# Optimization experiments

Hardware: AMD Instinct MI355X
Metric: run time of the kernel (lower is better)

Reference implementation:

```python
import jax, jax.numpy as jnp
import numpy as np

N, K, NB, C, L, H = 10000, 32, 64, 128, 3, 64  # atoms, neighbors, basis, channels, num l-orders, MLP hidden
AVG_AGGREGATE_NUM = 10.0
LN_EPS = 1e-5
MAX_ELEM = 300


def setup_inputs() -> dict:
    key = jax.random.key(0)
    ks = jax.random.split(key, 12)
    return {
        'atomic_numbers': jax.random.randint(ks[0], (N,), 0, MAX_ELEM),
        'edge_vec': jax.random.normal(ks[1], (N, K, 3), jnp.float32),
        'f_sparse_idx_node': jax.random.randint(ks[2], (N, K), 0, N),
        'attn_mask': jax.random.randint(ks[3], (N, K, 1), 0, 2) == 1,
        'edge_scalars': jax.random.normal(ks[4], (N, K, NB), jnp.float32),
        'src_emb': jax.random.normal(ks[5], (MAX_ELEM, NB), jnp.float32),
        'tgt_emb': jax.random.normal(ks[6], (MAX_ELEM, NB), jnp.float32),
        'W1': jax.random.normal(ks[7], (L, 3 * NB, H), jnp.float32) / np.sqrt(3 * NB),
        'b1': jnp.zeros((L, H), jnp.float32),
        'g1': jnp.ones((L, H), jnp.float32),
        'be1': jnp.zeros((L, H), jnp.float32),
        'W2': jax.random.normal(ks[8], (L, H, H), jnp.float32) / np.sqrt(H),
        'b2': jnp.zeros((L, H), jnp.float32),
        'g2': jnp.ones((L, H), jnp.float32),
        'be2': jnp.zeros((L, H), jnp.float32),
        'W3': jax.random.normal(ks[9], (L, H, C), jnp.float32) / np.sqrt(H),
        'b3': jnp.zeros((L, C), jnp.float32),
    }


def _layer_norm(x, g, b):
    mu = jnp.mean(x, axis=-1, keepdims=True)
    var = jnp.var(x, axis=-1, keepdims=True)
    return (x - mu) * jax.lax.rsqrt(var + LN_EPS) * g + b


def _sph_harmonics(unit):
    """e3nn real spherical harmonics l=0,1,2, normalization='norm' (unit input vecs)."""
    x, y, z = unit[..., 0], unit[..., 1], unit[..., 2]
    s3 = float(np.sqrt(3.0))
    y0 = jnp.ones_like(x)[..., None]                       # (N,K,1)
    y1 = jnp.stack([y, z, x], axis=-1)                      # (N,K,3)
    y2 = jnp.stack([s3 * x * y,
                    s3 * y * z,
                    0.5 * (3.0 * z * z - 1.0),
                    s3 * x * z,
                    0.5 * s3 * (x * x - y * y)], axis=-1)   # (N,K,5)
    return [y0, y1, y2]


def reference(atomic_numbers, edge_vec, f_sparse_idx_node, attn_mask, edge_scalars,
              src_emb, tgt_emb, W1, b1, g1, be1, W2, b2, g2, be2, W3, b3):
    n, k = edge_scalars.shape[:2]
    # gather atom-type embeddings: target per center atom, source per neighbor
    tgt = jnp.broadcast_to(tgt_emb[atomic_numbers][:, None, :], (n, k, tgt_emb.shape[1]))
    src = src_emb[atomic_numbers][f_sparse_idx_node]            # (N,K,NB)
    edge_dis_embed = jnp.concatenate([edge_scalars, tgt, src], axis=-1)  # (N,K,3*NB)

    unit = edge_vec / jnp.linalg.norm(edge_vec, axis=-1, keepdims=True)
    sh = _sph_harmonics(unit)

    feats = []
    for i in range(W1.shape[0]):  # small fixed loop over l = 0..lmax
        h = jax.nn.silu(_layer_norm(edge_dis_embed @ W1[i] + b1[i], g1[i], be1[i]))
        h = jax.nn.silu(_layer_norm(h @ W2[i] + b2[i], g2[i], be2[i]))
        h = h @ W3[i] + b3[i]                                   # (N,K,C)
        h = jnp.where(attn_mask, 0.0, h)                        # mask padded neighbors
        feats.append(jnp.einsum('mnd,mnh->mdh', sh[i], h))      # (N,2l+1,C)
    return jnp.concatenate(feats, axis=1) / AVG_AGGREGATE_NUM   # (N,9,C)
```

## Files before the change

kernel.cpp:

```cpp
#include <hip/hip_runtime.h>
#include <hip/hip_bf16.h>


typedef __attribute__((ext_vector_type(8))) short bf16x8;
typedef __attribute__((ext_vector_type(4))) short bf16x4;
typedef __attribute__((ext_vector_type(4))) float f32x4;

__device__ __forceinline__ unsigned short f2bf(float f) {
  __hip_bfloat16 h = __float2bfloat16(f);
  return *reinterpret_cast<unsigned short*>(&h);
}

__global__ __launch_bounds__(256) void prep_weights(
    const float* __restrict__ W1, const float* __restrict__ W2,
    const float* __restrict__ W3, unsigned short* __restrict__ wf) {
  int idx = blockIdx.x * 256 + threadIdx.x;
  if (idx >= 73728) return;
  float val;
  if (idx < 36864) {
    int l = idx / 12288, r = idx % 12288;
    int blk = r >> 9, e = r & 511;
    int Nt = blk / 6, Ks = blk % 6;
    int lane = e >> 3, j = e & 7;
    int k = Ks * 32 + (lane >> 4) * 8 + j;
    int nn = Nt * 16 + (lane & 15);
    val = W1[l * 192 * 64 + k * 64 + nn];
  } else if (idx < 49152) {
    int t = idx - 36864;
    int l = t / 4096, r = t % 4096;
    int blk = r >> 9, e = r & 511;
    int Nt = blk >> 1, Ks = blk & 1;
    int lane = e >> 3, j = e & 7;
    int k = Ks * 32 + (lane >> 4) * 8 + j;
    int nn = Nt * 16 + (lane & 15);
    val = W2[l * 64 * 64 + k * 64 + nn];
  } else {
    int t = idx - 49152;
    int l = t / 8192, r = t % 8192;
    int blk = r >> 9, e = r & 511;
    int Nt = blk >> 1, Ks = blk & 1;
    int lane = e >> 3, j = e & 7;
    int k = Ks * 32 + (lane >> 4) * 8 + j;
    int nn = Nt * 16 + (lane & 15);
    val = W3[l * 64 * 128 + k * 128 + nn];
  }
  wf[idx] = f2bf(val);
}

__global__ __launch_bounds__(256) void sniff_mask(const unsigned int* __restrict__ m,
                                                  int* __restrict__ flag) {
  __shared__ int cOther, cFloat;
  if (threadIdx.x == 0) { cOther = 0; cFloat = 0; }
  __syncthreads();
  int other = 0, flt = 0;
#pragma unroll
  for (int i = 0; i < 8; ++i) {
    unsigned int w = m[threadIdx.x * 8 + i];
    if (w == 0x3F800000u) flt++;
    else if (w > 1u) other++;
  }
  if (other) atomicAdd(&cOther, other);
  if (flt)   atomicAdd(&cFloat, flt);
  __syncthreads();
  if (threadIdx.x == 0) {
    int f;
    if (cOther == 0 && cFloat == 0) f = 0;
    else if (cFloat > cOther)       f = 2;
    else                            f = 1;
    *flag = f;
  }
}

__device__ __forceinline__ bf16x8 cvt8(float4 a, float4 b) {
  bf16x8 r;
  r[0] = (short)f2bf(a.x); r[1] = (short)f2bf(a.y);
  r[2] = (short)f2bf(a.z); r[3] = (short)f2bf(a.w);
  r[4] = (short)f2bf(b.x); r[5] = (short)f2bf(b.y);
  r[6] = (short)f2bf(b.z); r[7] = (short)f2bf(b.w);
  return r;
}

__device__ __forceinline__ void ln2(
    const f32x4 (&acc)[4][2], const float* __restrict__ bb,
    const float* __restrict__ gg, const float* __restrict__ be,
    unsigned short* Uw, int e, int g) {
  float v0[16], v1[16];
  float s0 = 0.f, s20 = 0.f, s1 = 0.f, s21 = 0.f;
#pragma unroll
  for (int mt = 0; mt < 4; ++mt) {
    float4 b4 = *reinterpret_cast<const float4*>(bb + mt * 16 + 4 * g);
    const float* b4p = reinterpret_cast<const float*>(&b4);
#pragma unroll
    for (int i = 0; i < 4; ++i) {
      float x0 = acc[mt][0][i] + b4p[i];
      float x1 = acc[mt][1][i] + b4p[i];
      v0[mt * 4 + i] = x0; s0 += x0; s20 += x0 * x0;
      v1[mt * 4 + i] = x1; s1 += x1; s21 += x1 * x1;
    }
  }
  s0 += __shfl_xor(s0, 16); s20 += __shfl_xor(s20, 16);
  s1 += __shfl_xor(s1, 16); s21 += __shfl_xor(s21, 16);
  s0 += __shfl_xor(s0, 32); s20 += __shfl_xor(s20, 32);
  s1 += __shfl_xor(s1, 32); s21 += __shfl_xor(s21, 32);
  float mu0 = s0 * 0.015625f, mu1 = s1 * 0.015625f;
  float r0 = rsqrtf(s20 * 0.015625f - mu0 * mu0 + 1e-5f);
  float r1 = rsqrtf(s21 * 0.015625f - mu1 * mu1 + 1e-5f);
#pragma unroll
  for (int mt = 0; mt < 4; ++mt) {
    float4 g4 = *reinterpret_cast<const float4*>(gg + mt * 16 + 4 * g);
    float4 e4 = *reinterpret_cast<const float4*>(be + mt * 16 + 4 * g);
    const float* g4p = reinterpret_cast<const float*>(&g4);
    const float* e4p = reinterpret_cast<const float*>(&e4);
    bf16x4 pk0, pk1;
#pragma unroll
    for (int i = 0; i < 4; ++i) {
      float y0 = (v0[mt * 4 + i] - mu0) * r0 * g4p[i] + e4p[i];
      float y1 = (v1[mt * 4 + i] - mu1) * r1 * g4p[i] + e4p[i];
      pk0[i] = (short)f2bf(y0 * __builtin_amdgcn_rcpf(1.0f + __expf(-y0)));
      pk1[i] = (short)f2bf(y1 * __builtin_amdgcn_rcpf(1.0f + __expf(-y1)));
    }
    *reinterpret_cast<bf16x4*>(Uw + e * 72 + mt * 16 + 4 * g) = pk0;
    *reinterpret_cast<bf16x4*>(Uw + (16 + e) * 72 + mt * 16 + 4 * g) = pk1;
  }
}

#define MFMA __builtin_amdgcn_mfma_f32_16x16x32_bf16

__global__ __launch_bounds__(256, 3) void edge_net_kernel(
    const int*   __restrict__ an_arr,
    const float* __restrict__ edge_vec,
    const int*   __restrict__ f_idx,
    const void*  __restrict__ attn_mask,
    const float* __restrict__ edge_scalars,
    const float* __restrict__ src_emb,
    const float* __restrict__ tgt_emb,
    const float* __restrict__ b1, const float* __restrict__ g1, const float* __restrict__ be1,
    const float* __restrict__ b2, const float* __restrict__ g2, const float* __restrict__ be2,
    const float* __restrict__ b3,
    const unsigned short* __restrict__ wf,
    const int* __restrict__ mask_flag,
    float* __restrict__ out, int Nat) {

  __shared__ __align__(16) unsigned short U[4][3200];

  const int tid  = threadIdx.x;
  const int wave = tid >> 6, lane = tid & 63;
  const int e = lane & 15, g = lane >> 4;
  int n = blockIdx.x * 4 + wave;
  const bool valid = (n < Nat);
  if (!valid) n = Nat - 1;

  unsigned short* Uw  = &U[wave][0];
  unsigned short* shB = Uw + 2560;

#pragma unroll
  for (int t = 0; t < 10; ++t) shB[t * 64 + lane] = 0;

  const int mflag = *mask_flag;
  if (g < 2) {
    int k = g * 16 + e;
    bool masked;
    if (mflag == 0)      masked = ((const int*)attn_mask)[n * 32 + k] != 0;
    else if (mflag == 1) masked = ((const unsigned char*)attn_mask)[n * 32 + k] != 0;
    else                 masked = ((const float*)attn_mask)[n * 32 + k] != 0.0f;
    const float mf = masked ? 0.0f : 1.0f;
    const float* ev = edge_vec + ((size_t)n * 32 + k) * 3;
    float ex = ev[0], ey = ev[1], ez = ev[2];
    float rn = rsqrtf(ex * ex + ey * ey + ez * ez);
    float x = ex * rn, y = ey * rn, z = ez * rn;
    const float s3 = 1.7320508075688772f;
    float s[9];
    s[0] = 1.f; s[1] = y; s[2] = z; s[3] = x;
    s[4] = s3 * x * y; s[5] = s3 * y * z; s[6] = 1.5f * z * z - 0.5f;
    s[7] = s3 * x * z; s[8] = 0.5f * s3 * (x * x - y * y);
#pragma unroll
    for (int d = 0; d < 9; ++d) shB[d * 40 + k] = f2bf(s[d] * mf);
  }

  const int an = an_arr[n];
  bf16x8 xf[2][6];
  {
    const float4* t0 = reinterpret_cast<const float4*>(tgt_emb + (size_t)an * 64 + g * 8);
    const float4* t1 = reinterpret_cast<const float4*>(tgt_emb + (size_t)an * 64 + 32 + g * 8);
    bf16x8 xt0 = cvt8(t0[0], t0[1]);
    bf16x8 xt1 = cvt8(t1[0], t1[1]);
#pragma unroll
    for (int nt = 0; nt < 2; ++nt) {
      int k = nt * 16 + e;
      const float* es = edge_scalars + ((size_t)n * 32 + k) * 64 + g * 8;
      const float4* p0 = reinterpret_cast<const float4*>(es);
      const float4* p1 = reinterpret_cast<const float4*>(es + 32);
      xf[nt][0] = cvt8(p0[0], p0[1]);
      xf[nt][1] = cvt8(p1[0], p1[1]);
      xf[nt][2] = xt0;
      xf[nt][3] = xt1;
      int srcA = an_arr[f_idx[n * 32 + k]];
      const float4* s0 = reinterpret_cast<const float4*>(src_emb + (size_t)srcA * 64 + g * 8);
      const float4* s1 = reinterpret_cast<const float4*>(src_emb + (size_t)srcA * 64 + 32 + g * 8);
      xf[nt][4] = cvt8(s0[0], s0[1]);
      xf[nt][5] = cvt8(s1[0], s1[1]);
    }
  }

  bf16x8 bfull = *reinterpret_cast<const bf16x8*>(shB + e * 40 + g * 8);

  for (int l = 0; l < 3; ++l) {
    const unsigned short* w1a = wf + l * 12288;
    const unsigned short* w2a = wf + 36864 + l * 4096;
    const unsigned short* w3a = wf + 49152 + l * 8192;

    f32x4 acc1[4][2];
#pragma unroll
    for (int mt = 0; mt < 4; ++mt)
#pragma unroll
      for (int nt = 0; nt < 2; ++nt) acc1[mt][nt] = (f32x4){0.f, 0.f, 0.f, 0.f};
#pragma unroll
    for (int mt = 0; mt < 4; ++mt)
#pragma unroll
      for (int ks = 0; ks < 6; ++ks) {
        bf16x8 wfr = *reinterpret_cast<const bf16x8*>(w1a + ((mt * 6 + ks) << 9) + lane * 8);
        acc1[mt][0] = MFMA(wfr, xf[0][ks], acc1[mt][0], 0, 0, 0);
        acc1[mt][1] = MFMA(wfr, xf[1][ks], acc1[mt][1], 0, 0, 0);
      }
    ln2(acc1, b1 + l * 64, g1 + l * 64, be1 + l * 64, Uw, e, g);

    bf16x8 hf[2][2];
#pragma unroll
    for (int nt = 0; nt < 2; ++nt)
#pragma unroll
      for (int ks = 0; ks < 2; ++ks)
        hf[nt][ks] = *reinterpret_cast<const bf16x8*>(Uw + (nt * 16 + e) * 72 + ks * 32 + g * 8);
    f32x4 acc2[4][2];
#pragma unroll
    for (int mt = 0; mt < 4; ++mt)
#pragma unroll
      for (int nt = 0; nt < 2; ++nt) acc2[mt][nt] = (f32x4){0.f, 0.f, 0.f, 0.f};
#pragma unroll
    for (int mt = 0; mt < 4; ++mt)
#pragma unroll
      for (int ks = 0; ks < 2; ++ks) {
        bf16x8 wfr = *reinterpret_cast<const bf16x8*>(w2a + ((mt * 2 + ks) << 9) + lane * 8);
        acc2[mt][0] = MFMA(wfr, hf[0][ks], acc2[mt][0], 0, 0, 0);
        acc2[mt][1] = MFMA(wfr, hf[1][ks], acc2[mt][1], 0, 0, 0);
      }
    ln2(acc2, b2 + l * 64, g2 + l * 64, be2 + l * 64, Uw, e, g);

#pragma unroll
    for (int nt = 0; nt < 2; ++nt)
#pragma unroll
      for (int ks = 0; ks < 2; ++ks)
        hf[nt][ks] = *reinterpret_cast<const bf16x8*>(Uw + (nt * 16 + e) * 72 + ks * 32 + g * 8);
    const float* b3l = b3 + l * 128;
    const int lo = l * l, hi = l * l + 2 * l;
    const bool dstore = valid && e >= lo && e <= hi;
    float* op = out + ((size_t)n * 9 + e) * 128 + 4 * g;
    bf16x8 bfr = (e >= lo && e <= hi) ? bfull : (bf16x8)(short)0;
#pragma unroll
    for (int half = 0; half < 2; ++half) {
#pragma unroll
      for (int mt = 0; mt < 4; ++mt) {
        const int mtg = half * 4 + mt;
        f32x4 a30 = (f32x4){0.f, 0.f, 0.f, 0.f};
        f32x4 a31 = (f32x4){0.f, 0.f, 0.f, 0.f};
#pragma unroll
        for (int ks = 0; ks < 2; ++ks) {
          bf16x8 wfr = *reinterpret_cast<const bf16x8*>(w3a + ((mtg * 2 + ks) << 9) + lane * 8);
          a30 = MFMA(wfr, hf[0][ks], a30, 0, 0, 0);
          a31 = MFMA(wfr, hf[1][ks], a31, 0, 0, 0);
        }
        float4 bb = *reinterpret_cast<const float4*>(b3l + mtg * 16 + 4 * g);
        const float* bbp = reinterpret_cast<const float*>(&bb);
#pragma unroll
        for (int i = 0; i < 4; ++i) {
          int row = (mt * 16 + 4 * g + i) * 40;
          Uw[row + e]      = f2bf(a30[i] + bbp[i]);
          Uw[row + 16 + e] = f2bf(a31[i] + bbp[i]);
        }
      }
      asm volatile("s_waitcnt lgkmcnt(0)" ::: "memory");
      __builtin_amdgcn_sched_barrier(0);
#pragma unroll
      for (int mt = 0; mt < 4; ++mt) {
        bf16x8 afr = *reinterpret_cast<const bf16x8*>(Uw + (mt * 16 + e) * 40 + g * 8);
        f32x4 ez = (f32x4){0.f, 0.f, 0.f, 0.f};
        ez = MFMA(afr, bfr, ez, 0, 0, 0);
        if (dstore) {
          float4 v;
          v.x = 0.1f * ez[0]; v.y = 0.1f * ez[1];
          v.z = 0.1f * ez[2]; v.w = 0.1f * ez[3];
          *reinterpret_cast<float4*>(op + (half * 4 + mt) * 16) = v;
        }
      }
      asm volatile("s_waitcnt lgkmcnt(0)" ::: "memory");
      __builtin_amdgcn_sched_barrier(0);
    }
  }
}

extern "C" void kernel_launch(void* const* d_in, const int* in_sizes, int n_in,
                              void* d_out, int out_size, void* d_ws, size_t ws_size,
                              hipStream_t stream) {
  const int*   atomic_numbers = (const int*)  d_in[0];
  const float* edge_vec       = (const float*)d_in[1];
  const int*   f_idx          = (const int*)  d_in[2];
  const void*  attn_mask      = d_in[3];
  const float* edge_scalars   = (const float*)d_in[4];
  const float* src_emb        = (const float*)d_in[5];
  const float* tgt_emb        = (const float*)d_in[6];
  const float* W1  = (const float*)d_in[7];
  const float* b1  = (const float*)d_in[8];
  const float* g1  = (const float*)d_in[9];
  const float* be1 = (const float*)d_in[10];
  const float* W2  = (const float*)d_in[11];
  const float* b2  = (const float*)d_in[12];
  const float* g2  = (const float*)d_in[13];
  const float* be2 = (const float*)d_in[14];
  const float* W3  = (const float*)d_in[15];
  const float* b3  = (const float*)d_in[16];

  unsigned short* wf = (unsigned short*)d_ws;
  int* mask_flag = ((int*)d_ws) + 36864;
  float* out = (float*)d_out;
  const int N = in_sizes[0];

  prep_weights<<<288, 256, 0, stream>>>(W1, W2, W3, wf);
  sniff_mask<<<1, 256, 0, stream>>>((const unsigned int*)attn_mask, mask_flag);
  edge_net_kernel<<<(N + 3) / 4, 256, 0, stream>>>(
      atomic_numbers, edge_vec, f_idx, attn_mask, edge_scalars,
      src_emb, tgt_emb, b1, g1, be1, b2, g2, be2, b3, wf, mask_flag, out, N);
}
```

Before: 150.6 us.

## Keep MLP hidden activations in registers via permuted weight K-layout

```diff
diff --git a/kernel.cpp b/kernel.cpp
--- a/kernel.cpp
+++ b/kernel.cpp
@@ -3,7 +3,6 @@
 
 
 typedef __attribute__((ext_vector_type(8))) short bf16x8;
-typedef __attribute__((ext_vector_type(4))) short bf16x4;
 typedef __attribute__((ext_vector_type(4))) float f32x4;
 
 __device__ __forceinline__ unsigned short f2bf(float f) {
@@ -26,23 +25,27 @@
     int nn = Nt * 16 + (lane & 15);
     val = W1[l * 192 * 64 + k * 64 + nn];
   } else if (idx < 49152) {
-    int t = idx - 36864;
-    int l = t / 4096, r = t % 4096;
+    int t2 = idx - 36864;
+    int l = t2 / 4096, r = t2 % 4096;
     int blk = r >> 9, e = r & 511;
     int Nt = blk >> 1, Ks = blk & 1;
     int lane = e >> 3, j = e & 7;
-    int k = Ks * 32 + (lane >> 4) * 8 + j;
+    int gg = lane >> 4;
+    int t = Ks * 8 + j;
+    int kk = 16 * (t >> 2) + 4 * gg + (t & 3);
     int nn = Nt * 16 + (lane & 15);
-    val = W2[l * 64 * 64 + k * 64 + nn];
+    val = W2[l * 64 * 64 + kk * 64 + nn];
   } else {
-    int t = idx - 49152;
-    int l = t / 8192, r = t % 8192;
+    int t2 = idx - 49152;
+    int l = t2 / 8192, r = t2 % 8192;
     int blk = r >> 9, e = r & 511;
     int Nt = blk >> 1, Ks = blk & 1;
     int lane = e >> 3, j = e & 7;
-    int k = Ks * 32 + (lane >> 4) * 8 + j;
+    int gg = lane >> 4;
+    int t = Ks * 8 + j;
+    int kk = 16 * (t >> 2) + 4 * gg + (t & 3);
     int nn = Nt * 16 + (lane & 15);
-    val = W3[l * 64 * 128 + k * 128 + nn];
+    val = W3[l * 64 * 128 + kk * 128 + nn];
   }
   wf[idx] = f2bf(val);
 }
@@ -83,7 +86,7 @@
 __device__ __forceinline__ void ln2(
     const f32x4 (&acc)[4][2], const float* __restrict__ bb,
     const float* __restrict__ gg, const float* __restrict__ be,
-    unsigned short* Uw, int e, int g) {
+    bf16x8 (&hfo)[2][2], int g) {
   float v0[16], v1[16];
   float s0 = 0.f, s20 = 0.f, s1 = 0.f, s21 = 0.f;
 #pragma unroll
@@ -111,16 +114,16 @@
     float4 e4 = *reinterpret_cast<const float4*>(be + mt * 16 + 4 * g);
     const float* g4p = reinterpret_cast<const float*>(&g4);
     const float* e4p = reinterpret_cast<const float*>(&e4);
-    bf16x4 pk0, pk1;
 #pragma unroll
     for (int i = 0; i < 4; ++i) {
       float y0 = (v0[mt * 4 + i] - mu0) * r0 * g4p[i] + e4p[i];
       float y1 = (v1[mt * 4 + i] - mu1) * r1 * g4p[i] + e4p[i];
-      pk0[i] = (short)f2bf(y0 * __builtin_amdgcn_rcpf(1.0f + __expf(-y0)));
-      pk1[i] = (short)f2bf(y1 * __builtin_amdgcn_rcpf(1.0f + __expf(-y1)));
+      float sl0 = y0 * __builtin_amdgcn_rcpf(1.0f + __expf(-y0));
+      float sl1 = y1 * __builtin_amdgcn_rcpf(1.0f + __expf(-y1));
+      const int t = mt * 4 + i;
+      hfo[0][t >> 3][t & 7] = (short)f2bf(sl0);
+      hfo[1][t >> 3][t & 7] = (short)f2bf(sl1);
     }
-    *reinterpret_cast<bf16x4*>(Uw + e * 72 + mt * 16 + 4 * g) = pk0;
-    *reinterpret_cast<bf16x4*>(Uw + (16 + e) * 72 + mt * 16 + 4 * g) = pk1;
   }
 }
 
@@ -152,6 +155,7 @@
 
   unsigned short* Uw  = &U[wave][0];
   unsigned short* shB = Uw + 2560;
+  unsigned int*   U32 = reinterpret_cast<unsigned int*>(Uw);
 
 #pragma unroll
   for (int t = 0; t < 10; ++t) shB[t * 64 + lane] = 0;
@@ -174,7 +178,7 @@
     s[4] = s3 * x * y; s[5] = s3 * y * z; s[6] = 1.5f * z * z - 0.5f;
     s[7] = s3 * x * z; s[8] = 0.5f * s3 * (x * x - y * y);
 #pragma unroll
-    for (int d = 0; d < 9; ++d) shB[d * 40 + k] = f2bf(s[d] * mf);
+    for (int d = 0; d < 9; ++d) shB[d * 40 + 2 * e + g] = f2bf(s[d] * mf);
   }
 
   const int an = an_arr[n];
@@ -222,14 +226,9 @@
         acc1[mt][0] = MFMA(wfr, xf[0][ks], acc1[mt][0], 0, 0, 0);
         acc1[mt][1] = MFMA(wfr, xf[1][ks], acc1[mt][1], 0, 0, 0);
       }
-    ln2(acc1, b1 + l * 64, g1 + l * 64, be1 + l * 64, Uw, e, g);
-
-    bf16x8 hf[2][2];
-#pragma unroll
-    for (int nt = 0; nt < 2; ++nt)
-#pragma unroll
-      for (int ks = 0; ks < 2; ++ks)
-        hf[nt][ks] = *reinterpret_cast<const bf16x8*>(Uw + (nt * 16 + e) * 72 + ks * 32 + g * 8);
+    bf16x8 hf1[2][2];
+    ln2(acc1, b1 + l * 64, g1 + l * 64, be1 + l * 64, hf1, g);
+
     f32x4 acc2[4][2];
 #pragma unroll
     for (int mt = 0; mt < 4; ++mt)
@@ -240,16 +239,12 @@
 #pragma unroll
       for (int ks = 0; ks < 2; ++ks) {
         bf16x8 wfr = *reinterpret_cast<const bf16x8*>(w2a + ((mt * 2 + ks) << 9) + lane * 8);
-        acc2[mt][0] = MFMA(wfr, hf[0][ks], acc2[mt][0], 0, 0, 0);
-        acc2[mt][1] = MFMA(wfr, hf[1][ks], acc2[mt][1], 0, 0, 0);
+        acc2[mt][0] = MFMA(wfr, hf1[0][ks], acc2[mt][0], 0, 0, 0);
+        acc2[mt][1] = MFMA(wfr, hf1[1][ks], acc2[mt][1], 0, 0, 0);
       }
-    ln2(acc2, b2 + l * 64, g2 + l * 64, be2 + l * 64, Uw, e, g);
-
-#pragma unroll
-    for (int nt = 0; nt < 2; ++nt)
-#pragma unroll
-      for (int ks = 0; ks < 2; ++ks)
-        hf[nt][ks] = *reinterpret_cast<const bf16x8*>(Uw + (nt * 16 + e) * 72 + ks * 32 + g * 8);
+    bf16x8 hf2[2][2];
+    ln2(acc2, b2 + l * 64, g2 + l * 64, be2 + l * 64, hf2, g);
+
     const float* b3l = b3 + l * 128;
     const int lo = l * l, hi = l * l + 2 * l;
     const bool dstore = valid && e >= lo && e <= hi;
@@ -265,16 +260,16 @@
 #pragma unroll
         for (int ks = 0; ks < 2; ++ks) {
           bf16x8 wfr = *reinterpret_cast<const bf16x8*>(w3a + ((mtg * 2 + ks) << 9) + lane * 8);
-          a30 = MFMA(wfr, hf[0][ks], a30, 0, 0, 0);
-          a31 = MFMA(wfr, hf[1][ks], a31, 0, 0, 0);
+          a30 = MFMA(wfr, hf2[0][ks], a30, 0, 0, 0);
+          a31 = MFMA(wfr, hf2[1][ks], a31, 0, 0, 0);
         }
         float4 bb = *reinterpret_cast<const float4*>(b3l + mtg * 16 + 4 * g);
         const float* bbp = reinterpret_cast<const float*>(&bb);
 #pragma unroll
         for (int i = 0; i < 4; ++i) {
-          int row = (mt * 16 + 4 * g + i) * 40;
-          Uw[row + e]      = f2bf(a30[i] + bbp[i]);
-          Uw[row + 16 + e] = f2bf(a31[i] + bbp[i]);
+          unsigned int pk = (unsigned int)f2bf(a30[i] + bbp[i])
+                          | ((unsigned int)f2bf(a31[i] + bbp[i]) << 16);
+          U32[(mt * 16 + 4 * g + i) * 20 + e] = pk;
         }
       }
       asm volatile("s_waitcnt lgkmcnt(0)" ::: "memory");
```

Result: no change. 153.0 us (+1.6%).
